# Kernel optimization log

Measured on AMD Instinct MI355X. Metric: run time of the kernel, lower is better.

## Reference

```python
import jax, jax.numpy as jnp
import numpy as np
import math

B, S, D, L, H, V, MAXP = 8, 512, 1024, 6, 8, 32000, 4096
HD = D // H
FF = 4 * D
EPS = 1e-5
SCALE = 1.0 / math.sqrt(HD)


def _ln(x, g, b):
    m = x.mean(-1, keepdims=True)
    xm = x - m
    v = (xm * xm).mean(-1, keepdims=True)
    return xm * jax.lax.rsqrt(v + EPS) * g + b


def setup_inputs() -> dict:
    key = jax.random.key(0)
    ks = jax.random.split(key, 16)
    std = 0.02
    inp = {
        'input_ids': jax.random.randint(ks[0], (B, S), 0, V, dtype=jnp.int32),
        'attention_mask': jnp.ones((B, S), dtype=jnp.int32),
        'current_position': 0,
        'tok_emb': jax.random.normal(ks[1], (V, D), jnp.float32) * std,
        'pos_emb': jax.random.normal(ks[2], (MAXP, D), jnp.float32) * std,
        'ln1_s': jnp.ones((L, D), jnp.float32),
        'ln1_b': jnp.zeros((L, D), jnp.float32),
        'Wq': jax.random.normal(ks[3], (L, D, D), jnp.float32) * std,
        'bq': jnp.zeros((L, D), jnp.float32),
        'Wk': jax.random.normal(ks[4], (L, D, D), jnp.float32) * std,
        'bk': jnp.zeros((L, D), jnp.float32),
        'Wv': jax.random.normal(ks[5], (L, D, D), jnp.float32) * std,
        'bv': jnp.zeros((L, D), jnp.float32),
        'Wo': jax.random.normal(ks[6], (L, D, D), jnp.float32) * std,
        'bo': jnp.zeros((L, D), jnp.float32),
        'ln2_s': jnp.ones((L, D), jnp.float32),
        'ln2_b': jnp.zeros((L, D), jnp.float32),
        'W1': jax.random.normal(ks[7], (L, D, FF), jnp.float32) * std,
        'b1': jnp.zeros((L, FF), jnp.float32),
        'W2': jax.random.normal(ks[8], (L, FF, D), jnp.float32) * std,
        'b2': jnp.zeros((L, D), jnp.float32),
        'lnf_s': jnp.ones((D,), jnp.float32),
        'lnf_b': jnp.zeros((D,), jnp.float32),
        'Wout': jax.random.normal(ks[9], (D, D), jnp.float32) * std,
        'bout': jnp.zeros((D,), jnp.float32),
    }
    return inp


def reference(input_ids, attention_mask, current_position, tok_emb, pos_emb,
              ln1_s, ln1_b, Wq, bq, Wk, bk, Wv, bv, Wo, bo,
              ln2_s, ln2_b, W1, b1, W2, b2, lnf_s, lnf_b, Wout, bout):
    pos = current_position + jnp.arange(S)  # [S]
    h = tok_emb[input_ids] + pos_emb[pos][None, :, :]  # [B,S,D]
    pad = (attention_mask == 0)[:, None, None, :]  # [B,1,1,S] key-padding mask

    def layer(h, p):
        (l1s, l1b, wq, bq_, wk, bk_, wv, bv_, wo, bo_,
         l2s, l2b, w1, b1_, w2, b2_) = p
        x = _ln(h, l1s, l1b)
        q = (x @ wq + bq_).reshape(B, S, H, HD).transpose(0, 2, 1, 3)
        k = (x @ wk + bk_).reshape(B, S, H, HD).transpose(0, 2, 1, 3)
        v = (x @ wv + bv_).reshape(B, S, H, HD).transpose(0, 2, 1, 3)
        scores = jnp.einsum('bhqd,bhkd->bhqk', q, k) * SCALE
        scores = jnp.where(pad, -10000.0, scores)
        attn = jax.nn.softmax(scores, axis=-1)
        o = jnp.einsum('bhqk,bhkd->bhqd', attn, v)
        o = o.transpose(0, 2, 1, 3).reshape(B, S, D)
        h = h + (o @ wo + bo_)
        x = _ln(h, l2s, l2b)
        mlp = jax.nn.gelu(x @ w1 + b1_, approximate=False) @ w2 + b2_
        return h + mlp, None

    h, _ = jax.lax.scan(layer, h, (ln1_s, ln1_b, Wq, bq, Wk, bk, Wv, bv, Wo, bo,
                                   ln2_s, ln2_b, W1, b1, W2, b2))
    h = _ln(h, lnf_s, lnf_b)
    return h @ Wout + bout
```

## Files before the change

kernel.cpp:

```cpp
#include <hip/hip_runtime.h>
#include <hip/hip_bf16.h>
#include <math.h>

#define BB 8
#define SS 512
#define DD 1024
#define LL 6
#define HH 8
#define HDD 128
#define FFF 4096
#define EPSF 1e-5f
#define SCALEF 0.08838834764831845f

typedef __attribute__((ext_vector_type(8))) _Float16 f16x8;
typedef __attribute__((ext_vector_type(4))) _Float16 f16x4;
typedef __attribute__((ext_vector_type(4))) float f32x4;

__device__ __forceinline__ void gload16(const void* g, void* l) {
  __builtin_amdgcn_global_load_lds(
      (const __attribute__((address_space(1))) void*)g,
      (__attribute__((address_space(3))) void*)l, 16, 0, 0);
}

__global__ __launch_bounds__(256, 3) void gemmk_kernel(
    const _Float16* __restrict__ Ag, const _Float16* __restrict__ Bg,
    const float* __restrict__ bias, void* __restrict__ outp,
    int Ndim, int Kdim, int Kstr, long zsA, long zsB, long zsOut, int emode) {
  __shared__ _Float16 lA[8192];
  __shared__ _Float16 lB[8192];
  const int tid = threadIdx.x;
  const int lane = tid & 63;
  const int wid = tid >> 6;
  const int z = blockIdx.z;
  const int m0 = blockIdx.y * 128;
  const int n0 = blockIdx.x * 128;
  const long K2 = (long)Kstr * 2;
  const char* Azc = (const char*)(Ag + (long)z * zsA + (long)m0 * Kstr);
  const char* Bzc = (const char*)(Bg + (long)z * zsB + (long)n0 * Kstr);

  const int wm = (wid >> 1) * 64;
  const int wn = (wid & 1) * 64;
  const int r16 = lane & 15;
  const int kq = lane >> 4;

  long roff[4];
#pragma unroll
  for (int i = 0; i < 4; ++i) {
    const int idx = tid + i * 256;
    const int r = idx >> 3;
    const int sc = ((idx & 7) << 4) ^ ((r & 7) << 4);
    roff[i] = (long)r * K2 + sc;
  }

  f32x4 acc[4][4];
#pragma unroll
  for (int mi = 0; mi < 4; ++mi)
#pragma unroll
    for (int ni = 0; ni < 4; ++ni) acc[mi][ni] = (f32x4){0.f, 0.f, 0.f, 0.f};

  const int nt = Kdim >> 6;
  for (int t = 0; t < nt; ++t) {
    const int kb = t << 7;
    __syncthreads();
#pragma unroll
    for (int i = 0; i < 4; ++i) {
      gload16(Azc + roff[i] + kb, (char*)lA + tid * 16 + i * 4096);
      gload16(Bzc + roff[i] + kb, (char*)lB + tid * 16 + i * 4096);
    }
    __syncthreads();
#pragma unroll
    for (int kk = 0; kk < 2; ++kk) {
      f16x8 af[4], bf[4];
#pragma unroll
      for (int mi = 0; mi < 4; ++mi) {
        const int R = wm + mi * 16 + r16;
        af[mi] = *(const f16x8*)((const char*)lA + R * 128 +
                                 ((kk * 64 + kq * 16) ^ ((R & 7) << 4)));
      }
#pragma unroll
      for (int ni = 0; ni < 4; ++ni) {
        const int R = wn + ni * 16 + r16;
        bf[ni] = *(const f16x8*)((const char*)lB + R * 128 +
                                 ((kk * 64 + kq * 16) ^ ((R & 7) << 4)));
      }
#pragma unroll
      for (int mi = 0; mi < 4; ++mi)
#pragma unroll
        for (int ni = 0; ni < 4; ++ni)
          acc[mi][ni] = __builtin_amdgcn_mfma_f32_16x16x32_f16(
              af[mi], bf[ni], acc[mi][ni], 0, 0, 0);
    }
  }

  _Float16* outH = (_Float16*)outp + (long)z * zsOut;
  const int rj = (lane >> 4) << 2;
  const long MSZq = (long)BB * SS * DD;
#pragma unroll
  for (int mi = 0; mi < 4; ++mi) {
#pragma unroll
    for (int ni = 0; ni < 4; ++ni) {
      const int col = n0 + wn + ni * 16 + r16;
#pragma unroll
      for (int j = 0; j < 4; ++j) {
        const int row = m0 + wm + mi * 16 + rj + j;
        float vv = acc[mi][ni][j];
        if (emode == 1) {
          vv += bias[col];
          int wsel = col >> 10, c = col & 1023;
          int b_ = row >> 9, s_ = row & 511;
          int hh = c >> 7, hd_ = c & 127;
          if (wsel < 2) {
            outH[wsel * MSZq + (((long)(b_ * HH + hh)) * SS + s_) * HDD + hd_] =
                (_Float16)vv;
          } else {
            outH[2 * MSZq + (((long)(b_ * HH + hh)) * HDD + hd_) * SS + s_] =
                (_Float16)vv;
          }
        } else if (emode == 5) {
          vv += bias[col];
          vv = 0.5f * vv * (1.0f + erff(vv * 0.70710678118654752f));
          outH[(long)row * Ndim + col] = (_Float16)vv;
        } else {
          outH[(long)row * Ndim + col] = (_Float16)vv;
        }
      }
    }
  }
}

__global__ __launch_bounds__(256) void flash_kernel(
    const _Float16* __restrict__ Qg, const _Float16* __restrict__ Kg,
    const _Float16* __restrict__ Vt, const int* __restrict__ amask,
    _Float16* __restrict__ xout) {
  __shared__ _Float16 Pl[4][32][136];
  __shared__ float rf_s[4][32];
  const int tid = threadIdx.x;
  const int lane = tid & 63;
  const int w = tid >> 6;
  const int bh = blockIdx.y;
  const int b_ = bh >> 3, hh = bh & 7;
  const int q0 = blockIdx.x * 128 + w * 32;
  const int r16 = lane & 15;
  const int kq = lane >> 4;
  const int rj = kq << 2;
  const _Float16* Qb = Qg + ((long)bh * SS + q0) * HDD;
  const _Float16* Kb = Kg + (long)bh * SS * HDD;
  const _Float16* Vb = Vt + (long)bh * HDD * SS;

  f16x8 qa[2][4];
#pragma unroll
  for (int mi = 0; mi < 2; ++mi)
#pragma unroll
    for (int kk = 0; kk < 4; ++kk)
      qa[mi][kk] = *(const f16x8*)(Qb + (long)(mi * 16 + r16) * HDD + kk * 32 +
                                   kq * 8);

  f32x4 acc[8][2];
#pragma unroll
  for (int mi = 0; mi < 8; ++mi)
#pragma unroll
    for (int ni = 0; ni < 2; ++ni) acc[mi][ni] = (f32x4){0.f, 0.f, 0.f, 0.f};
  float mrun[2][4], lrun[2][4];
#pragma unroll
  for (int mi = 0; mi < 2; ++mi)
#pragma unroll
    for (int j = 0; j < 4; ++j) {
      mrun[mi][j] = -INFINITY;
      lrun[mi][j] = 0.f;
    }

  for (int kt = 0; kt < 4; ++kt) {
    __syncthreads();
    const int s0 = kt * 128;
    int am[8];
#pragma unroll
    for (int ni = 0; ni < 8; ++ni)
      am[ni] = amask[b_ * SS + s0 + ni * 16 + r16];

    f32x4 sc[2][8];
#pragma unroll
    for (int mi = 0; mi < 2; ++mi)
#pragma unroll
      for (int ni = 0; ni < 8; ++ni) sc[mi][ni] = (f32x4){0.f, 0.f, 0.f, 0.f};
#pragma unroll
    for (int ni = 0; ni < 8; ++ni) {
      f16x8 kf[4];
#pragma unroll
      for (int kk = 0; kk < 4; ++kk)
        kf[kk] = *(const f16x8*)(Kb + (long)(s0 + ni * 16 + r16) * HDD +
                                 kk * 32 + kq * 8);
#pragma unroll
      for (int mi = 0; mi < 2; ++mi)
#pragma unroll
        for (int kk = 0; kk < 4; ++kk)
          sc[mi][ni] = __builtin_amdgcn_mfma_f32_16x16x32_f16(
              qa[mi][kk], kf[kk], sc[mi][ni], 0, 0, 0);
    }
#pragma unroll
    for (int mi = 0; mi < 2; ++mi)
#pragma unroll
      for (int ni = 0; ni < 8; ++ni)
#pragma unroll
        for (int j = 0; j < 4; ++j)
          sc[mi][ni][j] = am[ni] ? sc[mi][ni][j] * SCALEF : -10000.0f;

    float rf[2][4];
#pragma unroll
    for (int mi = 0; mi < 2; ++mi)
#pragma unroll
      for (int j = 0; j < 4; ++j) {
        float rm = -INFINITY;
#pragma unroll
        for (int ni = 0; ni < 8; ++ni) rm = fmaxf(rm, sc[mi][ni][j]);
#pragma unroll
        for (int off = 1; off < 16; off <<= 1)
          rm = fmaxf(rm, __shfl_xor(rm, off));
        const float mn = fmaxf(mrun[mi][j], rm);
        const float rfv = __expf(mrun[mi][j] - mn);
        mrun[mi][j] = mn;
        float rs = 0.f;
#pragma unroll
        for (int ni = 0; ni < 8; ++ni) {
          const float p = __expf(sc[mi][ni][j] - mn);
          sc[mi][ni][j] = p;
          rs += p;
        }
#pragma unroll
        for (int off = 1; off < 16; off <<= 1) rs += __shfl_xor(rs, off);
        lrun[mi][j] = lrun[mi][j] * rfv + rs;
        rf[mi][j] = rfv;
      }
    if (r16 == 0) {
#pragma unroll
      for (int mi = 0; mi < 2; ++mi)
#pragma unroll
        for (int j = 0; j < 4; ++j) rf_s[w][mi * 16 + rj + j] = rf[mi][j];
    }
#pragma unroll
    for (int mi = 0; mi < 2; ++mi)
#pragma unroll
      for (int ni = 0; ni < 8; ++ni)
#pragma unroll
        for (int j = 0; j < 4; ++j)
          Pl[w][mi * 16 + rj + j][ni * 16 + r16] = (_Float16)sc[mi][ni][j];
    __syncthreads();

    float rfq[2];
    rfq[0] = rf_s[w][r16];
    rfq[1] = rf_s[w][16 + r16];
#pragma unroll
    for (int mi2 = 0; mi2 < 8; ++mi2)
#pragma unroll
      for (int ni2 = 0; ni2 < 2; ++ni2)
#pragma unroll
        for (int j = 0; j < 4; ++j) acc[mi2][ni2][j] *= rfq[ni2];

    f16x8 pb[2][4];
#pragma unroll
    for (int ni2 = 0; ni2 < 2; ++ni2)
#pragma unroll
      for (int kk = 0; kk < 4; ++kk)
        pb[ni2][kk] =
            *(const f16x8*)(&Pl[w][ni2 * 16 + r16][kk * 32 + kq * 8]);
#pragma unroll
    for (int mi2 = 0; mi2 < 8; ++mi2) {
      f16x8 va[4];
#pragma unroll
      for (int kk = 0; kk < 4; ++kk)
        va[kk] = *(const f16x8*)(Vb + (long)(mi2 * 16 + r16) * SS + s0 +
                                 kk * 32 + kq * 8);
#pragma unroll
      for (int ni2 = 0; ni2 < 2; ++ni2)
#pragma unroll
        for (int kk = 0; kk < 4; ++kk)
          acc[mi2][ni2] = __builtin_amdgcn_mfma_f32_16x16x32_f16(
              va[kk], pb[ni2][kk], acc[mi2][ni2], 0, 0, 0);
    }
  }

  __syncthreads();
  if (r16 == 0) {
#pragma unroll
    for (int mi = 0; mi < 2; ++mi)
#pragma unroll
      for (int j = 0; j < 4; ++j)
        rf_s[w][mi * 16 + rj + j] = 1.0f / lrun[mi][j];
  }
  __syncthreads();
  float lq[2];
  lq[0] = rf_s[w][r16];
  lq[1] = rf_s[w][16 + r16];
#pragma unroll
  for (int mi2 = 0; mi2 < 8; ++mi2)
#pragma unroll
    for (int ni2 = 0; ni2 < 2; ++ni2) {
      f16x4 o;
#pragma unroll
      for (int j = 0; j < 4; ++j) o[j] = (_Float16)(acc[mi2][ni2][j] * lq[ni2]);
      const int qg = q0 + ni2 * 16 + r16;
      *(f16x4*)(&xout[((long)(b_ * SS + qg)) * DD + hh * HDD + mi2 * 16 + rj]) =
          o;
    }
}

__global__ __launch_bounds__(256) void reduce_ln_kernel(
    const _Float16* __restrict__ parts, int npart,
    const float* __restrict__ res, const float* __restrict__ bias,
    const float* __restrict__ lg, const float* __restrict__ lb,
    float* __restrict__ hout, _Float16* __restrict__ xout, long pzs) {
  const int row = blockIdx.x;
  const int c = threadIdx.x << 2;
  const long base = (long)row * DD + c;
  float4 a = *reinterpret_cast<const float4*>(&bias[c]);
  if (res) {
    const float4 r = *reinterpret_cast<const float4*>(&res[base]);
    a.x += r.x; a.y += r.y; a.z += r.z; a.w += r.w;
  }
  for (int p = 0; p < npart; ++p) {
    const f16x4 hpv = *reinterpret_cast<const f16x4*>(&parts[p * pzs + base]);
    a.x += (float)hpv[0]; a.y += (float)hpv[1];
    a.z += (float)hpv[2]; a.w += (float)hpv[3];
  }
  *reinterpret_cast<float4*>(&hout[base]) = a;
  if (!lg) return;
  float s = a.x + a.y + a.z + a.w;
  float ss = a.x * a.x + a.y * a.y + a.z * a.z + a.w * a.w;
#pragma unroll
  for (int off = 32; off; off >>= 1) {
    s += __shfl_down(s, off);
    ss += __shfl_down(ss, off);
  }
  __shared__ float red[8];
  const int wid = threadIdx.x >> 6, lane = threadIdx.x & 63;
  if (lane == 0) { red[wid] = s; red[4 + wid] = ss; }
  __syncthreads();
  if (threadIdx.x == 0) {
    s = red[0] + red[1] + red[2] + red[3];
    ss = red[4] + red[5] + red[6] + red[7];
    float mean = s * (1.0f / DD);
    float var = ss * (1.0f / DD) - mean * mean;
    red[0] = mean;
    red[1] = rsqrtf(var + EPSF);
  }
  __syncthreads();
  const float mean = red[0], rstd = red[1];
  const float4 gv = *reinterpret_cast<const float4*>(&lg[c]);
  const float4 bv = *reinterpret_cast<const float4*>(&lb[c]);
  f16x4 o;
  o[0] = (_Float16)((a.x - mean) * rstd * gv.x + bv.x);
  o[1] = (_Float16)((a.y - mean) * rstd * gv.y + bv.y);
  o[2] = (_Float16)((a.z - mean) * rstd * gv.z + bv.z);
  o[3] = (_Float16)((a.w - mean) * rstd * gv.w + bv.w);
  *reinterpret_cast<f16x4*>(&xout[base]) = o;
}

__global__ __launch_bounds__(256) void embed_ln_kernel(
    const int* __restrict__ ids, const int* __restrict__ curpos,
    const float* __restrict__ tok, const float* __restrict__ pos,
    const float* __restrict__ lg, const float* __restrict__ lb,
    float* __restrict__ h, _Float16* __restrict__ x) {
  const int rs = blockIdx.x;
  const int s_ = rs & (SS - 1);
  const int t = ids[rs];
  const int p = curpos[0] + s_;
  const int c = threadIdx.x << 2;
  const float4 tv = *reinterpret_cast<const float4*>(&tok[(long)t * DD + c]);
  const float4 pv = *reinterpret_cast<const float4*>(&pos[(long)p * DD + c]);
  float4 a = {tv.x + pv.x, tv.y + pv.y, tv.z + pv.z, tv.w + pv.w};
  *reinterpret_cast<float4*>(&h[(long)rs * DD + c]) = a;
  float s = a.x + a.y + a.z + a.w;
  float ss = a.x * a.x + a.y * a.y + a.z * a.z + a.w * a.w;
#pragma unroll
  for (int off = 32; off; off >>= 1) {
    s += __shfl_down(s, off);
    ss += __shfl_down(ss, off);
  }
  __shared__ float red[8];
  const int wid = threadIdx.x >> 6, lane = threadIdx.x & 63;
  if (lane == 0) { red[wid] = s; red[4 + wid] = ss; }
  __syncthreads();
  if (threadIdx.x == 0) {
    s = red[0] + red[1] + red[2] + red[3];
    ss = red[4] + red[5] + red[6] + red[7];
    float mean = s * (1.0f / DD);
    float var = ss * (1.0f / DD) - mean * mean;
    red[0] = mean;
    red[1] = rsqrtf(var + EPSF);
  }
  __syncthreads();
  const float mean = red[0], rstd = red[1];
  const float4 gv = *reinterpret_cast<const float4*>(&lg[c]);
  const float4 bv = *reinterpret_cast<const float4*>(&lb[c]);
  f16x4 o;
  o[0] = (_Float16)((a.x - mean) * rstd * gv.x + bv.x);
  o[1] = (_Float16)((a.y - mean) * rstd * gv.y + bv.y);
  o[2] = (_Float16)((a.z - mean) * rstd * gv.z + bv.z);
  o[3] = (_Float16)((a.w - mean) * rstd * gv.w + bv.w);
  *reinterpret_cast<f16x4*>(&x[(long)rs * DD + c]) = o;
}

#define SLABE 12582912L
__global__ __launch_bounds__(256) void wtransall_kernel(
    const float* __restrict__ Wq, const float* __restrict__ Wk,
    const float* __restrict__ Wv, const float* __restrict__ Wo,
    const float* __restrict__ W1, const float* __restrict__ W2, int lbase,
    long slabstride, _Float16* __restrict__ wall) {
  __shared__ float tt[64][65];
  const int id = blockIdx.x;
  const int lrel = id / 3072;
  const int l = lbase + lrel;
  int t = id % 3072;
  _Float16* slab = wall + (long)lrel * slabstride;
  const long lo = (long)l * DD * DD;
  const long lof = (long)l * DD * FFF;
  const float* src;
  _Float16* dst;
  int K, N;
  if (t < 1024) {
    const int wsel = t >> 8;
    t &= 255;
    src = (wsel == 0 ? Wq : wsel == 1 ? Wk : wsel == 2 ? Wv : Wo) + lo;
    dst = (wsel < 3) ? (slab + (long)wsel * DD * DD) : (slab + 3L * DD * DD);
    K = DD; N = DD;
  } else if (t < 2048) {
    t -= 1024; src = W1 + lof; dst = slab + 4L * DD * DD; K = DD; N = FFF;
  } else {
    t -= 2048; src = W2 + lof; dst = slab + 8L * DD * DD; K = FFF; N = DD;
  }
  const int ntile = N >> 6;
  const int n0 = (t % ntile) << 6;
  const int k0 = (t / ntile) << 6;
  const int tx = threadIdx.x & 63;
  const int ty = threadIdx.x >> 6;
#pragma unroll
  for (int i = 0; i < 16; ++i)
    tt[i * 4 + ty][tx] = src[(long)(k0 + i * 4 + ty) * N + n0 + tx];
  __syncthreads();
#pragma unroll
  for (int i = 0; i < 16; ++i) {
    const int r = i * 4 + ty;
    dst[(long)(n0 + r) * K + k0 + tx] = (_Float16)tt[tx][r];
  }
}

__global__ __launch_bounds__(256) void wtrans_kernel(
    const float* __restrict__ W, _Float16* __restrict__ WT, int K, int N) {
  __shared__ float tt[64][65];
  const int n0 = blockIdx.x * 64, k0 = blockIdx.y * 64;
  const int tx = threadIdx.x & 63;
  const int ty = threadIdx.x >> 6;
#pragma unroll
  for (int i = 0; i < 16; ++i)
    tt[i * 4 + ty][tx] = W[(long)(k0 + i * 4 + ty) * N + n0 + tx];
  __syncthreads();
#pragma unroll
  for (int i = 0; i < 16; ++i) {
    const int r = i * 4 + ty;
    WT[(long)(n0 + r) * K + k0 + tx] = (_Float16)tt[tx][r];
  }
}

__global__ __launch_bounds__(256) void packb_kernel(
    const float* __restrict__ bq, const float* __restrict__ bk,
    const float* __restrict__ bv, float* __restrict__ bqkv) {
  const int i = blockIdx.x * 256 + threadIdx.x;
  const int l = i / (3 * DD), j = i % (3 * DD);
  float v;
  if (j < DD) v = bq[l * DD + j];
  else if (j < 2 * DD) v = bk[l * DD + j - DD];
  else v = bv[l * DD + j - 2 * DD];
  bqkv[i] = v;
}

extern "C" void kernel_launch(void* const* d_in, const int* in_sizes, int n_in,
                              void* d_out, int out_size, void* d_ws,
                              size_t ws_size, hipStream_t stream) {
  const int* ids = (const int*)d_in[0];
  const int* amask = (const int*)d_in[1];
  const int* curp = (const int*)d_in[2];
  const float* tok = (const float*)d_in[3];
  const float* pose = (const float*)d_in[4];
  const float* ln1s = (const float*)d_in[5];
  const float* ln1b = (const float*)d_in[6];
  const float* Wq = (const float*)d_in[7];
  const float* bq = (const float*)d_in[8];
  const float* Wk = (const float*)d_in[9];
  const float* bk = (const float*)d_in[10];
  const float* Wv = (const float*)d_in[11];
  const float* bv = (const float*)d_in[12];
  const float* Wo = (const float*)d_in[13];
  const float* bo = (const float*)d_in[14];
  const float* ln2s = (const float*)d_in[15];
  const float* ln2b = (const float*)d_in[16];
  const float* W1 = (const float*)d_in[17];
  const float* b1 = (const float*)d_in[18];
  const float* W2 = (const float*)d_in[19];
  const float* b2 = (const float*)d_in[20];
  const float* lnfs = (const float*)d_in[21];
  const float* lnfb = (const float*)d_in[22];
  const float* Wout = (const float*)d_in[23];
  const float* bout = (const float*)d_in[24];

  const long MSZ = (long)BB * SS * DD;
  char* wsp = (char*)d_ws;
  float* h = (float*)wsp;
  _Float16* x = (_Float16*)(wsp + 16u * 1024 * 1024);
  _Float16* q = x + MSZ;
  _Float16* kb = q + MSZ;
  _Float16* vt = kb + MSZ;
  _Float16* big = vt + MSZ;
  _Float16* parts = big + MSZ * 4;
  float* bqkv = (float*)(parts + MSZ * 4);
  _Float16* wall = (_Float16*)((char*)bqkv + 128 * 1024);
  const size_t base_b = (size_t)((char*)wall - wsp);
  const bool prepack =
      ws_size >= base_b + (size_t)(6 * SLABE + (long)DD * DD) * 2 + 4096;
  const int nslab = prepack ? 6 : 1;
  _Float16* woutT = wall + (long)nslab * SLABE;

  const int M = BB * SS;
  dim3 blk(256);
  const long pzs = (long)M * DD;

  embed_ln_kernel<<<M, blk, 0, stream>>>(ids, curp, tok, pose, ln1s, ln1b, h, x);
  packb_kernel<<<(LL * 3 * DD) / 256, blk, 0, stream>>>(bq, bk, bv, bqkv);
  wtrans_kernel<<<dim3(DD / 64, DD / 64), blk, 0, stream>>>(Wout, woutT, DD, DD);
  if (prepack)
    wtransall_kernel<<<6 * 3072, blk, 0, stream>>>(Wq, Wk, Wv, Wo, W1, W2, 0,
                                                   SLABE, wall);

  const dim3 gQKV(3 * DD / 128, M / 128, 1);
  const dim3 gFA(SS / 128, BB * HH);
  const dim3 gF1(FFF / 128, M / 128, 1);
  const dim3 gK2(DD / 128, M / 128, 2);
  const dim3 gK4(DD / 128, M / 128, 4);

  for (int l = 0; l < LL; ++l) {
    _Float16* slab = wall + (long)(prepack ? l : 0) * SLABE;
    _Float16* qkvT = slab;
    _Float16* woT = slab + 3L * DD * DD;
    _Float16* w1T = slab + 4L * DD * DD;
    _Float16* w2T = slab + 8L * DD * DD;
    if (!prepack)
      wtransall_kernel<<<3072, blk, 0, stream>>>(Wq, Wk, Wv, Wo, W1, W2, l, 0,
                                                 wall);
    gemmk_kernel<<<gQKV, blk, 0, stream>>>(x, qkvT, bqkv + l * 3 * DD, q,
                                           3 * DD, DD, DD, 0, 0, 0, 1);
    flash_kernel<<<gFA, blk, 0, stream>>>(q, kb, vt, amask, x);
    gemmk_kernel<<<gK2, blk, 0, stream>>>(x, woT, nullptr, parts, DD, DD / 2,
                                          DD, DD / 2, DD / 2, pzs, 6);
    reduce_ln_kernel<<<M, blk, 0, stream>>>(parts, 2, h, bo + l * DD,
                                            ln2s + l * DD, ln2b + l * DD, h, x,
                                            pzs);
    gemmk_kernel<<<gF1, blk, 0, stream>>>(x, w1T, b1 + l * FFF, big, FFF, DD,
                                          DD, 0, 0, 0, 5);
    gemmk_kernel<<<gK4, blk, 0, stream>>>(big, w2T, nullptr, parts, DD,
                                          FFF / 4, FFF, FFF / 4, FFF / 4, pzs,
                                          6);
    const float* ng = (l < LL - 1) ? (ln1s + (l + 1) * DD) : lnfs;
    const float* nb = (l < LL - 1) ? (ln1b + (l + 1) * DD) : lnfb;
    reduce_ln_kernel<<<M, blk, 0, stream>>>(parts, 4, h, b2 + l * DD, ng, nb,
                                            h, x, pzs);
  }
  gemmk_kernel<<<gK2, blk, 0, stream>>>(x, woutT, nullptr, parts, DD, DD / 2,
                                        DD, DD / 2, DD / 2, pzs, 6);
  reduce_ln_kernel<<<M, blk, 0, stream>>>(parts, 2, nullptr, bout, nullptr,
                                          nullptr, (float*)d_out, nullptr, pzs);
}
```

Measured before the change: 1.600 ms.

## Template GEMM launch bounds, split-K 4 for Wo/Wout, vectorize weight transpose

Templates the GEMM kernel on its min-blocks-per-CU launch bound and uses 4 for the FF1, FF2, Wo and Wout GEMMs while QKV stays at 3. The Wo and final output projections move from split-K 2 to split-K 4, giving more blocks to fill the CUs, and the reductions now sum 4 partials. The weight transpose is rewritten to use float4 loads and 8-wide half stores through a shared helper. Risks are register spills from the tighter launch bound and extra partial-sum traffic from the wider split.

After: 1.638 ms. 2.3% more time.

```diff
diff --git a/kernel.cpp b/kernel.cpp
--- a/kernel.cpp
+++ b/kernel.cpp
@@ -22,7 +22,8 @@
       (__attribute__((address_space(3))) void*)l, 16, 0, 0);
 }
 
-__global__ __launch_bounds__(256, 3) void gemmk_kernel(
+template <int MAXB>
+__global__ __launch_bounds__(256, MAXB) void gemmk_kernel(
     const _Float16* __restrict__ Ag, const _Float16* __restrict__ Bg,
     const float* __restrict__ bias, void* __restrict__ outp,
     int Ndim, int Kdim, int Kstr, long zsA, long zsB, long zsOut, int emode) {
@@ -399,13 +400,40 @@
   *reinterpret_cast<f16x4*>(&x[(long)rs * DD + c]) = o;
 }
 
+__device__ __forceinline__ void ttile(const float* __restrict__ src,
+                                      _Float16* __restrict__ dst, int K, int N,
+                                      int k0, int n0) {
+  __shared__ float tt[64][65];
+  const int tx = threadIdx.x;
+#pragma unroll
+  for (int it = 0; it < 4; ++it) {
+    const int r = it * 16 + (tx >> 4);
+    const int cc = (tx & 15) << 2;
+    const float4 v =
+        *reinterpret_cast<const float4*>(&src[(long)(k0 + r) * N + n0 + cc]);
+    tt[r][cc] = v.x;
+    tt[r][cc + 1] = v.y;
+    tt[r][cc + 2] = v.z;
+    tt[r][cc + 3] = v.w;
+  }
+  __syncthreads();
+#pragma unroll
+  for (int it = 0; it < 2; ++it) {
+    const int rr = it * 32 + (tx >> 3);
+    const int cc = (tx & 7) << 3;
+    f16x8 o;
+#pragma unroll
+    for (int e = 0; e < 8; ++e) o[e] = (_Float16)tt[cc + e][rr];
+    *reinterpret_cast<f16x8*>(&dst[(long)(n0 + rr) * K + k0 + cc]) = o;
+  }
+}
+
 #define SLABE 12582912L
 __global__ __launch_bounds__(256) void wtransall_kernel(
     const float* __restrict__ Wq, const float* __restrict__ Wk,
     const float* __restrict__ Wv, const float* __restrict__ Wo,
     const float* __restrict__ W1, const float* __restrict__ W2, int lbase,
     long slabstride, _Float16* __restrict__ wall) {
-  __shared__ float tt[64][65];
   const int id = blockIdx.x;
   const int lrel = id / 3072;
   const int l = lbase + lrel;
@@ -428,36 +456,12 @@
     t -= 2048; src = W2 + lof; dst = slab + 8L * DD * DD; K = FFF; N = DD;
   }
   const int ntile = N >> 6;
-  const int n0 = (t % ntile) << 6;
-  const int k0 = (t / ntile) << 6;
-  const int tx = threadIdx.x & 63;
-  const int ty = threadIdx.x >> 6;
-#pragma unroll
-  for (int i = 0; i < 16; ++i)
-    tt[i * 4 + ty][tx] = src[(long)(k0 + i * 4 + ty) * N + n0 + tx];
-  __syncthreads();
-#pragma unroll
-  for (int i = 0; i < 16; ++i) {
-    const int r = i * 4 + ty;
-    dst[(long)(n0 + r) * K + k0 + tx] = (_Float16)tt[tx][r];
-  }
+  ttile(src, dst, K, N, (t / ntile) << 6, (t % ntile) << 6);
 }
 
 __global__ __launch_bounds__(256) void wtrans_kernel(
     const float* __restrict__ W, _Float16* __restrict__ WT, int K, int N) {
-  __shared__ float tt[64][65];
-  const int n0 = blockIdx.x * 64, k0 = blockIdx.y * 64;
-  const int tx = threadIdx.x & 63;
-  const int ty = threadIdx.x >> 6;
-#pragma unroll
-  for (int i = 0; i < 16; ++i)
-    tt[i * 4 + ty][tx] = W[(long)(k0 + i * 4 + ty) * N + n0 + tx];
-  __syncthreads();
-#pragma unroll
-  for (int i = 0; i < 16; ++i) {
-    const int r = i * 4 + ty;
-    WT[(long)(n0 + r) * K + k0 + tx] = (_Float16)tt[tx][r];
-  }
+  ttile(W, WT, K, N, blockIdx.y << 6, blockIdx.x << 6);
 }
 
 __global__ __launch_bounds__(256) void packb_kernel(
@@ -532,7 +536,6 @@
   const dim3 gQKV(3 * DD / 128, M / 128, 1);
   const dim3 gFA(SS / 128, BB * HH);
   const dim3 gF1(FFF / 128, M / 128, 1);
-  const dim3 gK2(DD / 128, M / 128, 2);
   const dim3 gK4(DD / 128, M / 128, 4);
 
   for (int l = 0; l < LL; ++l) {
@@ -544,26 +547,27 @@
     if (!prepack)
       wtransall_kernel<<<3072, blk, 0, stream>>>(Wq, Wk, Wv, Wo, W1, W2, l, 0,
                                                  wall);
-    gemmk_kernel<<<gQKV, blk, 0, stream>>>(x, qkvT, bqkv + l * 3 * DD, q,
-                                           3 * DD, DD, DD, 0, 0, 0, 1);
+    gemmk_kernel<3><<<gQKV, blk, 0, stream>>>(x, qkvT, bqkv + l * 3 * DD, q,
+                                              3 * DD, DD, DD, 0, 0, 0, 1);
     flash_kernel<<<gFA, blk, 0, stream>>>(q, kb, vt, amask, x);
-    gemmk_kernel<<<gK2, blk, 0, stream>>>(x, woT, nullptr, parts, DD, DD / 2,
-                                          DD, DD / 2, DD / 2, pzs, 6);
-    reduce_ln_kernel<<<M, blk, 0, stream>>>(parts, 2, h, bo + l * DD,
+    gemmk_kernel<4><<<gK4, blk, 0, stream>>>(x, woT, nullptr, parts, DD,
+                                             DD / 4, DD, DD / 4, DD / 4, pzs,
+                                             6);
+    reduce_ln_kernel<<<M, blk, 0, stream>>>(parts, 4, h, bo + l * DD,
                                             ln2s + l * DD, ln2b + l * DD, h, x,
                                             pzs);
-    gemmk_kernel<<<gF1, blk, 0, stream>>>(x, w1T, b1 + l * FFF, big, FFF, DD,
-                                          DD, 0, 0, 0, 5);
-    gemmk_kernel<<<gK4, blk, 0, stream>>>(big, w2T, nullptr, parts, DD,
-                                          FFF / 4, FFF, FFF / 4, FFF / 4, pzs,
-                                          6);
+    gemmk_kernel<4><<<gF1, blk, 0, stream>>>(x, w1T, b1 + l * FFF, big, FFF,
+                                             DD, DD, 0, 0, 0, 5);
+    gemmk_kernel<4><<<gK4, blk, 0, stream>>>(big, w2T, nullptr, parts, DD,
+                                             FFF / 4, FFF, FFF / 4, FFF / 4,
+                                             pzs, 6);
     const float* ng = (l < LL - 1) ? (ln1s + (l + 1) * DD) : lnfs;
     const float* nb = (l < LL - 1) ? (ln1b + (l + 1) * DD) : lnfb;
     reduce_ln_kernel<<<M, blk, 0, stream>>>(parts, 4, h, b2 + l * DD, ng, nb,
                                             h, x, pzs);
   }
-  gemmk_kernel<<<gK2, blk, 0, stream>>>(x, woutT, nullptr, parts, DD, DD / 2,
-                                        DD, DD / 2, DD / 2, pzs, 6);
-  reduce_ln_kernel<<<M, blk, 0, stream>>>(parts, 2, nullptr, bout, nullptr,
+  gemmk_kernel<4><<<gK4, blk, 0, stream>>>(x, woutT, nullptr, parts, DD,
+                                           DD / 4, DD, DD / 4, DD / 4, pzs, 6);
+  reduce_ln_kernel<<<M, blk, 0, stream>>>(parts, 4, nullptr, bout, nullptr,
                                           nullptr, (float*)d_out, nullptr, pzs);
 }
```
